# Kernel optimization log

Measured on AMD Instinct MI355X. Metric: run time of the kernel, lower is better.

Reference implementation:

```python
import jax, jax.numpy as jnp
import numpy as np

N_CONST = 1.0
M_CONST = 11008.0

def setup_inputs() -> dict:
    key = jax.random.key(0)
    ks = jax.random.split(key, 7)
    N, LM_D, GNN_D, H = 131072, 1024, 200, 128
    lm_embeds = jax.random.normal(ks[0], (N, LM_D), dtype=jnp.float32)
    gnn_embeds = jax.random.normal(ks[1], (N, GNN_D), dtype=jnp.float32)
    neg_gnn_embeds = jax.random.normal(ks[2], (N, GNN_D), dtype=jnp.float32)
    lm_W = jax.random.normal(ks[3], (LM_D, H), dtype=jnp.float32) * (1.0 / np.sqrt(LM_D))
    lm_b = jnp.zeros((H,), dtype=jnp.float32)
    gnn_W = jax.random.normal(ks[4], (GNN_D, H), dtype=jnp.float32) * (1.0 / np.sqrt(GNN_D))
    gnn_b = jnp.zeros((H,), dtype=jnp.float32)
    return {"lm_embeds": lm_embeds, "gnn_embeds": gnn_embeds,
            "neg_gnn_embeds": neg_gnn_embeds,
            "lm_W": lm_W, "lm_b": lm_b, "gnn_W": gnn_W, "gnn_b": gnn_b}

def _l2norm(x):
    return x / jnp.linalg.norm(x, axis=-1, keepdims=True)

def _cal(lm_in, gnn_in, lm_W, lm_b, gnn_W, gnn_b, neg):
    l = _l2norm(lm_in @ lm_W + lm_b)       # [N, H]
    g = _l2norm(gnn_in @ gnn_W + gnn_b)    # [N, H]
    # diagonal of l @ g.T == per-row dot product (avoids NxN matmul)
    logits = jnp.exp(jnp.sum(l * g, axis=-1))  # [N]
    ratio = logits / (logits + N_CONST / M_CONST)
    return jnp.log(1.0 - ratio) if neg else jnp.log(ratio)

def reference(lm_embeds, gnn_embeds, neg_gnn_embeds, lm_W, lm_b, gnn_W, gnn_b):
    pos = jnp.mean(_cal(lm_embeds, gnn_embeds, lm_W, lm_b, gnn_W, gnn_b, False))
    neg = jnp.mean(_cal(lm_embeds, neg_gnn_embeds, lm_W, lm_b, gnn_W, gnn_b, True))
    return -pos - neg
```

## Files before the change

### kernel.cpp

```cpp
#include <hip/hip_runtime.h>
#include <hip/hip_bf16.h>
#include <stdint.h>

#define NROWS 131072
#define LMD   1024
#define GNND  200
#define HD    128
#define BLOCK 256
#define MTILE 64
#define NBLK  (NROWS/MTILE)
#define WCH   16384

typedef __attribute__((ext_vector_type(4))) float  f32x4;
typedef __attribute__((ext_vector_type(8))) short  bf16x8;

#define GLDS(SRC, DST) __builtin_amdgcn_global_load_lds( \
    (const __attribute__((address_space(1))) unsigned int*)(SRC), \
    (__attribute__((address_space(3))) unsigned int*)(DST), 16, 0, 0)
#define SCHED0  __builtin_amdgcn_sched_barrier(0)
#define BAR     __builtin_amdgcn_s_barrier()
#define VMW(N)  asm volatile("s_waitcnt vmcnt(" #N ")" ::: "memory")

__device__ __forceinline__ short f2bf(float x) {
    union { __hip_bfloat16 h; short s; } u;
    u.h = __float2bfloat16(x);
    return u.s;
}

__device__ __forceinline__ bf16x8 cvt8(f32x4 a, f32x4 b) {
    bf16x8 r;
    r[0]=f2bf(a[0]); r[1]=f2bf(a[1]); r[2]=f2bf(a[2]); r[3]=f2bf(a[3]);
    r[4]=f2bf(b[0]); r[5]=f2bf(b[1]); r[6]=f2bf(b[2]); r[7]=f2bf(b[3]);
    return r;
}

__device__ __forceinline__ float red16(float v) {
    #pragma unroll
    for (int m=1; m<16; m<<=1) v += __shfl_xor(v, m, 16);
    return v;
}

__global__ void prep_weights(const float* __restrict__ lm_W,
                             const float* __restrict__ gnn_W,
                             short* __restrict__ W1S, short* __restrict__ W2S)
{
    int idx = blockIdx.x*BLOCK + threadIdx.x;
    int row = (idx >> 6) & 127;
    int e   = idx & 63;
    int kk  = (idx >> 13)*64 + (e ^ ((row & 7)*8));
    W1S[idx] = f2bf(lm_W[(long)kk*HD + row]);
    if (idx < 4*8192) {
        W2S[idx] = (kk < GNND) ? f2bf(gnn_W[(long)kk*HD + row]) : (short)0;
    }
}

__global__ __launch_bounds__(BLOCK) void fused(
    const float* __restrict__ lm,  const float* __restrict__ gnn,
    const float* __restrict__ ngn,
    const float* __restrict__ lm_b, const float* __restrict__ gnn_b,
    const char* __restrict__ W1S,  const char* __restrict__ W2S,
    float* __restrict__ partials)
{
    __shared__ short lbuf[4*8192];
    __shared__ float sp[4], sn[4];

    const int tid  = threadIdx.x;
    const int lane = tid & 63;
    const int win  = tid >> 6;
    const int col  = lane & 15;
    const int g    = lane >> 4;
    const int wq   = win*4096 + lane*16;
    const long row = (long)blockIdx.x * MTILE + win*16 + col;
    const int rotg = blockIdx.x & 7;

    const char* aL = (const char*)lm  + row*(LMD*4L)  + g*32;
    const char* aG = (const char*)gnn + row*(GNND*4L) + g*32;
    const char* aN = (const char*)ngn + row*(GNND*4L) + g*32;
    const char* clampG = (const char*)gnn + (size_t)NROWS*GNND*4 - 16;
    const char* clampN = (const char*)ngn + (size_t)NROWS*GNND*4 - 16;

    const float CC   = 1.0f / 11008.0f;
    const float LOGC = -9.3063777f;
    const f32x4 fz = {0.f,0.f,0.f,0.f};

    auto LOFF = [&](int p)->int { return ((p + rotg) & 7) * 512; };
    auto WSRC = [&](int p)->const char* {
        if (p < 16) {
            int lc = 2*(((p >> 1) + rotg) & 7) + (p & 1);
            return W1S + (size_t)lc*WCH;
        }
        return W2S + (size_t)(p - 16)*WCH;
    };

    auto ISSUEW = [&](const char* ws, int b) {
        const char* s = ws + wq;
        char* d = (char*)lbuf + (size_t)b*WCH + wq;
        #pragma unroll
        for (int i=0;i<4;i++) GLDS(s + i*1024, d + i*1024);
    };
    auto LOADG = [&](const char* base, int off, const char* cl, f32x4 (&S)[8]) {
        #pragma unroll
        for (int j=0;j<4;j++) {
            const char* p0 = base + off + j*128;
            const char* p1 = p0 + 16;
            if (cl) { if (p0 > cl) p0 = cl;  if (p1 > cl) p1 = cl; }
            S[2*j]   = *(const f32x4*)p0;
            S[2*j+1] = *(const f32x4*)p1;
        }
    };
    auto COMP = [&](int c, int half, f32x4 (&S)[8], f32x4 (&acc)[8]) {
        const short* wb = lbuf + (c & 3)*8192 + col*64;
        const int sw = (col & 7)*8;
        #pragma unroll
        for (int ks=0; ks<2; ++ks) {
            bf16x8 af = cvt8(S[half*4 + 2*ks], S[half*4 + 2*ks + 1]);
            const short* cb = wb + ((ks*32 + g*8) ^ sw);
            #pragma unroll
            for (int t=0;t<8;t++) {
                bf16x8 wf = *(const bf16x8*)(cb + t*1024);
                acc[t] = __builtin_amdgcn_mfma_f32_16x16x32_bf16(af, wf, acc[t], 0,0,0);
            }
        }
    };

    f32x4 accL[8], accG[8];
    #pragma unroll
    for (int t=0;t<8;t++) accL[t] = fz;
    f32x4 SA[8], SB[8];
    float pos_acc = 0.f, neg_acc = 0.f;

    float bl[8], bg[8];
    #pragma unroll
    for (int t=0;t<8;t++) bl[t] = lm_b[t*16+col];
    #pragma unroll
    for (int t=0;t<8;t++) bg[t] = gnn_b[t*16+col];
    SCHED0;
    ISSUEW(WSRC(0), 0); ISSUEW(WSRC(1), 1); ISSUEW(WSRC(2), 2);
    LOADG(aL, LOFF(0), nullptr, SA);
    LOADG(aL, LOFF(1), nullptr, SB);
    SCHED0; VMW(24); SCHED0; BAR; SCHED0;
    #pragma unroll
    for (int t=0;t<8;t++) { asm volatile("" : "+v"(bl[t])); asm volatile("" : "+v"(bg[t])); }

    #pragma unroll
    for (int gg=0; gg<8; ++gg) {
        f32x4 (&S)[8] = (gg & 1) ? SB : SA;
        ISSUEW(WSRC(2*gg+3), (2*gg+3) & 3);
        SCHED0;
        COMP(2*gg, 0, S, accL);
        SCHED0; VMW(16); SCHED0; BAR; SCHED0;
        ISSUEW(WSRC(2*gg+4), (2*gg+4) & 3);
        SCHED0;
        COMP(2*gg+1, 1, S, accL);
        SCHED0;
        if (gg < 6)       LOADG(aL, LOFF(gg+2), nullptr, S);
        else if (gg == 6) LOADG(aG,   0, clampG, S);
        else              LOADG(aG, 512, clampG, S);
        SCHED0; VMW(24); SCHED0; BAR; SCHED0;
    }

    #pragma unroll
    for (int t=0;t<8;t++) {
        #pragma unroll
        for (int r=0;r<4;r++) accL[t][r] += bl[t];
    }
    #pragma unroll
    for (int t=0;t<8;t++) accG[t] = fz;

    ISSUEW(WSRC(19), 3);
    SCHED0;
    COMP(16, 0, SA, accG);
    SCHED0; VMW(16); SCHED0; BAR; SCHED0;

    COMP(17, 1, SA, accG);
    SCHED0;
    LOADG(aN, 0, clampN, SA);
    SCHED0; VMW(20); SCHED0; BAR; SCHED0;

    COMP(18, 0, SB, accG);
    SCHED0; VMW(8); SCHED0; BAR; SCHED0;

    COMP(19, 1, SB, accG);
    SCHED0;
    LOADG(aN, 512, clampN, SB);
    SCHED0;

    #pragma unroll
    for (int r=0;r<4;r++) {
        float lg=0.f, ll=0.f, gg2=0.f;
        #pragma unroll
        for (int t=0;t<8;t++) {
            float lv=accL[t][r], gv=accG[t][r]+bg[t];
            lg += lv*gv; ll += lv*lv; gg2 += gv*gv;
        }
        lg=red16(lg); ll=red16(ll); gg2=red16(gg2);
        float d  = lg * rsqrtf(ll*gg2);
        float pi = d - logf(expf(d)+CC);
        if (col==0) pos_acc += pi;
    }
    #pragma unroll
    for (int t=0;t<8;t++) accG[t] = fz;

    COMP(20, 0, SA, accG);
    COMP(21, 1, SA, accG);
    COMP(22, 0, SB, accG);
    COMP(23, 1, SB, accG);

    #pragma unroll
    for (int r=0;r<4;r++) {
        float ln=0.f, nn=0.f, ll=0.f;
        #pragma unroll
        for (int t=0;t<8;t++) {
            float lv=accL[t][r], nv=accG[t][r]+bg[t];
            ln += lv*nv; nn += nv*nv; ll += lv*lv;
        }
        ln=red16(ln); nn=red16(nn); ll=red16(ll);
        float d  = ln * rsqrtf(ll*nn);
        float ni = LOGC - logf(expf(d)+CC);
        if (col==0) neg_acc += ni;
    }

    #pragma unroll
    for (int m=1;m<64;m<<=1) {
        pos_acc += __shfl_xor(pos_acc, m, 64);
        neg_acc += __shfl_xor(neg_acc, m, 64);
    }
    if (lane==0) { sp[win]=pos_acc; sn[win]=neg_acc; }
    __syncthreads();
    if (tid==0) {
        float p=0.f,n=0.f;
        #pragma unroll
        for (int w=0;w<4;w++){ p+=sp[w]; n+=sn[w]; }
        partials[blockIdx.x*2]   = p;
        partials[blockIdx.x*2+1] = n;
    }
}

__global__ void finalize(const float* __restrict__ partials, float* __restrict__ out)
{
    __shared__ float sp[BLOCK], sn[BLOCK];
    float p=0.f, n=0.f;
    for (int i=threadIdx.x; i<NBLK; i+=BLOCK) { p += partials[2*i]; n += partials[2*i+1]; }
    sp[threadIdx.x]=p; sn[threadIdx.x]=n;
    __syncthreads();
    for (int s=BLOCK/2; s>0; s>>=1) {
        if (threadIdx.x < s) { sp[threadIdx.x]+=sp[threadIdx.x+s]; sn[threadIdx.x]+=sn[threadIdx.x+s]; }
        __syncthreads();
    }
    if (threadIdx.x==0) out[0] = -(sp[0]+sn[0]) / (float)NROWS;
}

extern "C" void kernel_launch(void* const* d_in, const int* in_sizes, int n_in,
                              void* d_out, int out_size, void* d_ws, size_t ws_size,
                              hipStream_t stream)
{
    const float* lm    = (const float*)d_in[0];
    const float* gnn   = (const float*)d_in[1];
    const float* ngn   = (const float*)d_in[2];
    const float* lm_W  = (const float*)d_in[3];
    const float* lm_b  = (const float*)d_in[4];
    const float* gnn_W = (const float*)d_in[5];
    const float* gnn_b = (const float*)d_in[6];

    short* W1S = (short*)d_ws;
    short* W2S = (short*)((char*)d_ws + 262144);
    float* partials = (float*)((char*)d_ws + 262144 + 65536);

    prep_weights<<<512, BLOCK, 0, stream>>>(lm_W, gnn_W, W1S, W2S);
    fused<<<NBLK, BLOCK, 0, stream>>>(lm, gnn, ngn, lm_b, gnn_b,
                                      (const char*)W1S, (const char*)W2S, partials);
    finalize<<<1, BLOCK, 0, stream>>>(partials, (float*)d_out);
}
```

Before: 178.5 us.

## Make fused kernel persistent over four row tiles with paired weight-chunk pipeline

```diff
diff --git a/kernel.cpp b/kernel.cpp
--- a/kernel.cpp
+++ b/kernel.cpp
@@ -8,7 +8,8 @@
 #define HD    128
 #define BLOCK 256
 #define MTILE 64
-#define NBLK  (NROWS/MTILE)
+#define GRID  512
+#define NTILE 4
 #define WCH   16384
 
 typedef __attribute__((ext_vector_type(4))) float  f32x4;
@@ -54,7 +55,7 @@
     }
 }
 
-__global__ __launch_bounds__(BLOCK) void fused(
+__global__ __launch_bounds__(BLOCK, 2) void fused(
     const float* __restrict__ lm,  const float* __restrict__ gnn,
     const float* __restrict__ ngn,
     const float* __restrict__ lm_b, const float* __restrict__ gnn_b,
@@ -70,27 +71,20 @@
     const int col  = lane & 15;
     const int g    = lane >> 4;
     const int wq   = win*4096 + lane*16;
-    const long row = (long)blockIdx.x * MTILE + win*16 + col;
-    const int rotg = blockIdx.x & 7;
-
-    const char* aL = (const char*)lm  + row*(LMD*4L)  + g*32;
-    const char* aG = (const char*)gnn + row*(GNND*4L) + g*32;
-    const char* aN = (const char*)ngn + row*(GNND*4L) + g*32;
+
+    const long rowoff = (long)((long)blockIdx.x*MTILE + win*16 + col);
+    const long TSL = (long)GRID*MTILE*(LMD*4L);
+    const long TSG = (long)GRID*MTILE*(GNND*4L);
+
+    const char* aL = (const char*)lm  + rowoff*(LMD*4L)  + g*32;
+    const char* aG = (const char*)gnn + rowoff*(GNND*4L) + g*32;
+    const char* aN = (const char*)ngn + rowoff*(GNND*4L) + g*32;
     const char* clampG = (const char*)gnn + (size_t)NROWS*GNND*4 - 16;
     const char* clampN = (const char*)ngn + (size_t)NROWS*GNND*4 - 16;
 
     const float CC   = 1.0f / 11008.0f;
     const float LOGC = -9.3063777f;
     const f32x4 fz = {0.f,0.f,0.f,0.f};
-
-    auto LOFF = [&](int p)->int { return ((p + rotg) & 7) * 512; };
-    auto WSRC = [&](int p)->const char* {
-        if (p < 16) {
-            int lc = 2*(((p >> 1) + rotg) & 7) + (p & 1);
-            return W1S + (size_t)lc*WCH;
-        }
-        return W2S + (size_t)(p - 16)*WCH;
-    };
 
     auto ISSUEW = [&](const char* ws, int b) {
         const char* s = ws + wq;
@@ -108,9 +102,16 @@
             S[2*j+1] = *(const f32x4*)p1;
         }
     };
-    auto COMP = [&](int c, int half, f32x4 (&S)[8], f32x4 (&acc)[8]) {
+
+    f32x4 SA[8], SB[8];
+    f32x4 accL[8], accG[8];
+    float pos_acc = 0.f, neg_acc = 0.f;
+
+    auto COMP = [&](int c, f32x4 (&acc)[8]) {
         const short* wb = lbuf + (c & 3)*8192 + col*64;
         const int sw = (col & 7)*8;
+        f32x4 (&S)[8] = ((c>>1)&1) ? SB : SA;
+        const int half = c & 1;
         #pragma unroll
         for (int ks=0; ks<2; ++ks) {
             bf16x8 af = cvt8(S[half*4 + 2*ks], S[half*4 + 2*ks + 1]);
@@ -122,12 +123,10 @@
             }
         }
     };
-
-    f32x4 accL[8], accG[8];
-    #pragma unroll
-    for (int t=0;t<8;t++) accL[t] = fz;
-    f32x4 SA[8], SB[8];
-    float pos_acc = 0.f, neg_acc = 0.f;
+    auto WPAIR = [&](int S)->const char* {
+        if (S < 8)  return W1S + (size_t)(2*S)*WCH;
+        return (S & 1) ? (W2S + 2*WCH) : W2S;
+    };
 
     float bl[8], bg[8];
     #pragma unroll
@@ -135,89 +134,124 @@
     #pragma unroll
     for (int t=0;t<8;t++) bg[t] = gnn_b[t*16+col];
     SCHED0;
-    ISSUEW(WSRC(0), 0); ISSUEW(WSRC(1), 1); ISSUEW(WSRC(2), 2);
-    LOADG(aL, LOFF(0), nullptr, SA);
-    LOADG(aL, LOFF(1), nullptr, SB);
-    SCHED0; VMW(24); SCHED0; BAR; SCHED0;
+
+    ISSUEW(W1S,        0);
+    ISSUEW(W1S + WCH,  1);
+    LOADG(aL, 0, nullptr, SA);
+    SCHED0;
+    ISSUEW(W1S + 2*WCH, 2);
+    ISSUEW(W1S + 3*WCH, 3);
+    LOADG(aL, 512, nullptr, SB);
+    SCHED0; VMW(16); SCHED0; BAR; SCHED0;
     #pragma unroll
     for (int t=0;t<8;t++) { asm volatile("" : "+v"(bl[t])); asm volatile("" : "+v"(bg[t])); }
 
-    #pragma unroll
-    for (int gg=0; gg<8; ++gg) {
-        f32x4 (&S)[8] = (gg & 1) ? SB : SA;
-        ISSUEW(WSRC(2*gg+3), (2*gg+3) & 3);
-        SCHED0;
-        COMP(2*gg, 0, S, accL);
-        SCHED0; VMW(16); SCHED0; BAR; SCHED0;
-        ISSUEW(WSRC(2*gg+4), (2*gg+4) & 3);
-        SCHED0;
-        COMP(2*gg+1, 1, S, accL);
-        SCHED0;
-        if (gg < 6)       LOADG(aL, LOFF(gg+2), nullptr, S);
-        else if (gg == 6) LOADG(aG,   0, clampG, S);
-        else              LOADG(aG, 512, clampG, S);
-        SCHED0; VMW(24); SCHED0; BAR; SCHED0;
-    }
-
-    #pragma unroll
-    for (int t=0;t<8;t++) {
-        #pragma unroll
-        for (int r=0;r<4;r++) accL[t][r] += bl[t];
-    }
-    #pragma unroll
-    for (int t=0;t<8;t++) accG[t] = fz;
-
-    ISSUEW(WSRC(19), 3);
-    SCHED0;
-    COMP(16, 0, SA, accG);
-    SCHED0; VMW(16); SCHED0; BAR; SCHED0;
-
-    COMP(17, 1, SA, accG);
-    SCHED0;
-    LOADG(aN, 0, clampN, SA);
-    SCHED0; VMW(20); SCHED0; BAR; SCHED0;
-
-    COMP(18, 0, SB, accG);
-    SCHED0; VMW(8); SCHED0; BAR; SCHED0;
-
-    COMP(19, 1, SB, accG);
-    SCHED0;
-    LOADG(aN, 512, clampN, SB);
-    SCHED0;
-
-    #pragma unroll
-    for (int r=0;r<4;r++) {
-        float lg=0.f, ll=0.f, gg2=0.f;
+    #pragma unroll 1
+    for (int t4 = 0; t4 < NTILE; ++t4) {
+        const bool last = (t4 == NTILE-1);
+
+        #pragma unroll
+        for (int t=0;t<8;t++) accL[t] = fz;
+
+        #pragma unroll
+        for (int S = 0; S < 7; ++S) {
+            const char* wp = WPAIR(S+1);
+            ISSUEW(wp,       ((S+1)&1)*2    );
+            ISSUEW(wp + WCH, ((S+1)&1)*2 + 1);
+            SCHED0;
+            COMP(2*S,   accL);
+            COMP(2*S+1, accL);
+            SCHED0;
+            if (S < 6) LOADG(aL, (S+2)*512, nullptr, (S&1) ? SB : SA);
+            else       LOADG(aG, 0, clampG, SA);
+            SCHED0; VMW(8); SCHED0; BAR; SCHED0;
+        }
+        ISSUEW(W2S,       0);
+        ISSUEW(W2S + WCH, 1);
+        SCHED0;
+        COMP(14, accL);
+        COMP(15, accL);
+        SCHED0;
+        LOADG(aG, 512, clampG, SB);
+        SCHED0; VMW(8); SCHED0; BAR; SCHED0;
+
         #pragma unroll
         for (int t=0;t<8;t++) {
-            float lv=accL[t][r], gv=accG[t][r]+bg[t];
-            lg += lv*gv; ll += lv*lv; gg2 += gv*gv;
-        }
-        lg=red16(lg); ll=red16(ll); gg2=red16(gg2);
-        float d  = lg * rsqrtf(ll*gg2);
-        float pi = d - logf(expf(d)+CC);
-        if (col==0) pos_acc += pi;
-    }
-    #pragma unroll
-    for (int t=0;t<8;t++) accG[t] = fz;
-
-    COMP(20, 0, SA, accG);
-    COMP(21, 1, SA, accG);
-    COMP(22, 0, SB, accG);
-    COMP(23, 1, SB, accG);
-
-    #pragma unroll
-    for (int r=0;r<4;r++) {
-        float ln=0.f, nn=0.f, ll=0.f;
-        #pragma unroll
-        for (int t=0;t<8;t++) {
-            float lv=accL[t][r], nv=accG[t][r]+bg[t];
-            ln += lv*nv; nn += nv*nv; ll += lv*lv;
-        }
-        ln=red16(ln); nn=red16(nn); ll=red16(ll);
-        float d  = ln * rsqrtf(ll*nn);
-        float ni = LOGC - logf(expf(d)+CC);
-        if (col==0) neg_acc += ni;
+            #pragma unroll
+            for (int r=0;r<4;r++) accL[t][r] += bl[t];
+        }
+        #pragma unroll
+        for (int t=0;t<8;t++) accG[t] = fz;
+
+        ISSUEW(W2S + 2*WCH, 2);
+        ISSUEW(W2S + 3*WCH, 3);
+        SCHED0;
+        COMP(16, accG);
+        COMP(17, accG);
+        SCHED0;
+        LOADG(aN, 0, clampN, SA);
+        SCHED0; VMW(8); SCHED0; BAR; SCHED0;
+
+        COMP(18, accG);
+        COMP(19, accG);
+        SCHED0;
+        LOADG(aN, 512, clampN, SB);
+        SCHED0; VMW(8); SCHED0; BAR; SCHED0;
+
+        #pragma unroll
+        for (int r=0;r<4;r++) {
+            float lg=0.f, ll=0.f, gg2=0.f;
+            #pragma unroll
+            for (int t=0;t<8;t++) {
+                float lv=accL[t][r], gv=accG[t][r]+bg[t];
+                lg += lv*gv; ll += lv*lv; gg2 += gv*gv;
+            }
+            lg=red16(lg); ll=red16(ll); gg2=red16(gg2);
+            float d  = lg * rsqrtf(ll*gg2);
+            float pi = d - logf(expf(d)+CC);
+            if (col==0) pos_acc += pi;
+        }
+        #pragma unroll
+        for (int t=0;t<8;t++) accG[t] = fz;
+
+        COMP(20, accG);
+        COMP(21, accG);
+        SCHED0;
+        if (!last) {
+            LOADG(aL + TSL, 0, nullptr, SA);
+            SCHED0; VMW(8); SCHED0; BAR; SCHED0;
+        } else {
+            SCHED0; VMW(0); SCHED0; BAR; SCHED0;
+        }
+
+        if (!last) {
+            ISSUEW(W1S,       0);
+            ISSUEW(W1S + WCH, 1);
+            SCHED0;
+        }
+        COMP(22, accG);
+        COMP(23, accG);
+        SCHED0;
+        if (!last) {
+            LOADG(aL + TSL, 512, nullptr, SB);
+            SCHED0; VMW(8); SCHED0; BAR; SCHED0;
+        }
+
+        #pragma unroll
+        for (int r=0;r<4;r++) {
+            float ln=0.f, nn=0.f, ll=0.f;
+            #pragma unroll
+            for (int t=0;t<8;t++) {
+                float lv=accL[t][r], nv=accG[t][r]+bg[t];
+                ln += lv*nv; nn += nv*nv; ll += lv*lv;
+            }
+            ln=red16(ln); nn=red16(nn); ll=red16(ll);
+            float d  = ln * rsqrtf(ll*nn);
+            float ni = LOGC - logf(expf(d)+CC);
+            if (col==0) neg_acc += ni;
+        }
+
+        aL += TSL; aG += TSG; aN += TSG;
     }
 
     #pragma unroll
@@ -240,7 +274,7 @@
 {
     __shared__ float sp[BLOCK], sn[BLOCK];
     float p=0.f, n=0.f;
-    for (int i=threadIdx.x; i<NBLK; i+=BLOCK) { p += partials[2*i]; n += partials[2*i+1]; }
+    for (int i=threadIdx.x; i<GRID; i+=BLOCK) { p += partials[2*i]; n += partials[2*i+1]; }
     sp[threadIdx.x]=p; sn[threadIdx.x]=n;
     __syncthreads();
     for (int s=BLOCK/2; s>0; s>>=1) {
@@ -267,7 +301,7 @@
     float* partials = (float*)((char*)d_ws + 262144 + 65536);
 
     prep_weights<<<512, BLOCK, 0, stream>>>(lm_W, gnn_W, W1S, W2S);
-    fused<<<NBLK, BLOCK, 0, stream>>>(lm, gnn, ngn, lm_b, gnn_b,
+    fused<<<GRID, BLOCK, 0, stream>>>(lm, gnn, ngn, lm_b, gnn_b,
                                       (const char*)W1S, (const char*)W2S, partials);
     finalize<<<1, BLOCK, 0, stream>>>(partials, (float*)d_out);
 }
```

Result: slower. 296.1 us (+65.9%).

## Split output columns across wave pairs with 32-row tiles and LDS cross-wave reduction

Applied to the files above, without the earlier changes.

```diff
diff --git a/kernel.cpp b/kernel.cpp
--- a/kernel.cpp
+++ b/kernel.cpp
@@ -7,7 +7,7 @@
 #define GNND  200
 #define HD    128
 #define BLOCK 256
-#define MTILE 64
+#define MTILE 32
 #define NBLK  (NROWS/MTILE)
 #define WCH   16384
 
@@ -20,6 +20,7 @@
 #define SCHED0  __builtin_amdgcn_sched_barrier(0)
 #define BAR     __builtin_amdgcn_s_barrier()
 #define VMW(N)  asm volatile("s_waitcnt vmcnt(" #N ")" ::: "memory")
+#define LGKM0   asm volatile("s_waitcnt lgkmcnt(0)" ::: "memory")
 
 __device__ __forceinline__ short f2bf(float x) {
     union { __hip_bfloat16 h; short s; } u;
@@ -62,6 +63,8 @@
     float* __restrict__ partials)
 {
     __shared__ short lbuf[4*8192];
+    __shared__ float esumP[2][32][3];
+    __shared__ float esumN[2][32][3];
     __shared__ float sp[4], sn[4];
 
     const int tid  = threadIdx.x;
@@ -69,8 +72,12 @@
     const int win  = tid >> 6;
     const int col  = lane & 15;
     const int g    = lane >> 4;
+    const int rowg = win & 1;
+    const int colg = win >> 1;
+    const int colbase = colg*64;
     const int wq   = win*4096 + lane*16;
-    const long row = (long)blockIdx.x * MTILE + win*16 + col;
+    const long R0  = (long)blockIdx.x * MTILE;
+    const long row = R0 + rowg*16 + col;
     const int rotg = blockIdx.x & 7;
 
     const char* aL = (const char*)lm  + row*(LMD*4L)  + g*32;
@@ -108,39 +115,39 @@
             S[2*j+1] = *(const f32x4*)p1;
         }
     };
-    auto COMP = [&](int c, int half, f32x4 (&S)[8], f32x4 (&acc)[8]) {
-        const short* wb = lbuf + (c & 3)*8192 + col*64;
+    auto COMP = [&](int c, int half, f32x4 (&S)[8], f32x4 (&acc)[4]) {
+        const short* wb = lbuf + (c & 3)*8192 + (colbase + col)*64;
         const int sw = (col & 7)*8;
         #pragma unroll
         for (int ks=0; ks<2; ++ks) {
             bf16x8 af = cvt8(S[half*4 + 2*ks], S[half*4 + 2*ks + 1]);
             const short* cb = wb + ((ks*32 + g*8) ^ sw);
             #pragma unroll
-            for (int t=0;t<8;t++) {
+            for (int t=0;t<4;t++) {
                 bf16x8 wf = *(const bf16x8*)(cb + t*1024);
                 acc[t] = __builtin_amdgcn_mfma_f32_16x16x32_bf16(af, wf, acc[t], 0,0,0);
             }
         }
     };
 
-    f32x4 accL[8], accG[8];
-    #pragma unroll
-    for (int t=0;t<8;t++) accL[t] = fz;
+    f32x4 accL[4], accG[4];
+    #pragma unroll
+    for (int t=0;t<4;t++) accL[t] = fz;
     f32x4 SA[8], SB[8];
     float pos_acc = 0.f, neg_acc = 0.f;
 
-    float bl[8], bg[8];
-    #pragma unroll
-    for (int t=0;t<8;t++) bl[t] = lm_b[t*16+col];
-    #pragma unroll
-    for (int t=0;t<8;t++) bg[t] = gnn_b[t*16+col];
+    float bl[4], bg[4];
+    #pragma unroll
+    for (int t=0;t<4;t++) bl[t] = lm_b[colbase + t*16 + col];
+    #pragma unroll
+    for (int t=0;t<4;t++) bg[t] = gnn_b[colbase + t*16 + col];
     SCHED0;
     ISSUEW(WSRC(0), 0); ISSUEW(WSRC(1), 1); ISSUEW(WSRC(2), 2);
     LOADG(aL, LOFF(0), nullptr, SA);
     LOADG(aL, LOFF(1), nullptr, SB);
     SCHED0; VMW(24); SCHED0; BAR; SCHED0;
     #pragma unroll
-    for (int t=0;t<8;t++) { asm volatile("" : "+v"(bl[t])); asm volatile("" : "+v"(bg[t])); }
+    for (int t=0;t<4;t++) { asm volatile("" : "+v"(bl[t])); asm volatile("" : "+v"(bg[t])); }
 
     #pragma unroll
     for (int gg=0; gg<8; ++gg) {
@@ -160,12 +167,12 @@
     }
 
     #pragma unroll
-    for (int t=0;t<8;t++) {
+    for (int t=0;t<4;t++) {
         #pragma unroll
         for (int r=0;r<4;r++) accL[t][r] += bl[t];
     }
     #pragma unroll
-    for (int t=0;t<8;t++) accG[t] = fz;
+    for (int t=0;t<4;t++) accG[t] = fz;
 
     ISSUEW(WSRC(19), 3);
     SCHED0;
@@ -189,17 +196,27 @@
     for (int r=0;r<4;r++) {
         float lg=0.f, ll=0.f, gg2=0.f;
         #pragma unroll
-        for (int t=0;t<8;t++) {
+        for (int t=0;t<4;t++) {
             float lv=accL[t][r], gv=accG[t][r]+bg[t];
             lg += lv*gv; ll += lv*lv; gg2 += gv*gv;
         }
         lg=red16(lg); ll=red16(ll); gg2=red16(gg2);
+        if (col==0) {
+            int rr = rowg*16 + g*4 + r;
+            esumP[colg][rr][0]=lg; esumP[colg][rr][1]=ll; esumP[colg][rr][2]=gg2;
+        }
+    }
+    SCHED0; LGKM0; SCHED0; BAR; SCHED0;
+    if (win < 2 && lane < 16) {
+        int rr = rowg*16 + lane;
+        float lg  = esumP[0][rr][0] + esumP[1][rr][0];
+        float ll  = esumP[0][rr][1] + esumP[1][rr][1];
+        float gg2 = esumP[0][rr][2] + esumP[1][rr][2];
         float d  = lg * rsqrtf(ll*gg2);
-        float pi = d - logf(expf(d)+CC);
-        if (col==0) pos_acc += pi;
-    }
-    #pragma unroll
-    for (int t=0;t<8;t++) accG[t] = fz;
+        pos_acc = d - logf(expf(d)+CC);
+    }
+    #pragma unroll
+    for (int t=0;t<4;t++) accG[t] = fz;
 
     COMP(20, 0, SA, accG);
     COMP(21, 1, SA, accG);
@@ -210,14 +227,24 @@
     for (int r=0;r<4;r++) {
         float ln=0.f, nn=0.f, ll=0.f;
         #pragma unroll
-        for (int t=0;t<8;t++) {
+        for (int t=0;t<4;t++) {
             float lv=accL[t][r], nv=accG[t][r]+bg[t];
             ln += lv*nv; nn += nv*nv; ll += lv*lv;
         }
         ln=red16(ln); nn=red16(nn); ll=red16(ll);
+        if (col==0) {
+            int rr = rowg*16 + g*4 + r;
+            esumN[colg][rr][0]=ln; esumN[colg][rr][1]=nn; esumN[colg][rr][2]=ll;
+        }
+    }
+    SCHED0; LGKM0; SCHED0; BAR; SCHED0;
+    if (win < 2 && lane < 16) {
+        int rr = rowg*16 + lane;
+        float ln = esumN[0][rr][0] + esumN[1][rr][0];
+        float nn = esumN[0][rr][1] + esumN[1][rr][1];
+        float ll = esumN[0][rr][2] + esumN[1][rr][2];
         float d  = ln * rsqrtf(ll*nn);
-        float ni = LOGC - logf(expf(d)+CC);
-        if (col==0) neg_acc += ni;
+        neg_acc = LOGC - logf(expf(d)+CC);
     }
 
     #pragma unroll
```

Measured after the change: 274.7 us. 1.54x slower.
